# Optimization experiments

Hardware: AMD Instinct MI355X
Metric: run time of the kernel (lower is better)

## Reference

```python
import jax, jax.numpy as jnp
import numpy as np

K = 16          # neighbors per node
EPS = 1e-5      # BatchNorm eps
BN_SCALE = 1.0 / np.sqrt(1.0 + EPS)  # eval BN with running mean=0, var=1


def _knn_idx(x, k):
    # x: [B, N, d] -> idx [B, N, k] of k nearest neighbors (self excluded)
    sq = jnp.sum(x * x, axis=-1)                               # [B, N]
    d2 = sq[:, :, None] + sq[:, None, :] - 2.0 * jnp.einsum('bnd,bmd->bnm', x, x)
    n = x.shape[1]
    d2 = jnp.where(jnp.eye(n, dtype=bool)[None], jnp.inf, d2)  # no self loops
    _, idx = jax.lax.top_k(-d2, k)
    return idx


def _edge_conv(x, idx, W, b, g, be):
    # PyG EdgeConv: max_j MLP([x_i, x_j - x_i]); MLP = Linear+BN(eval)+ReLU
    xj = jax.vmap(lambda xb, ib: xb[ib])(x, idx)               # [B, N, k, d]
    xi = x[:, :, None, :]
    m = jnp.concatenate([jnp.broadcast_to(xi, xj.shape), xj - xi], axis=-1)
    h = m @ W + b                                              # [B, N, k, out]
    h = g * (h * BN_SCALE) + be                                # eval BatchNorm
    h = jax.nn.relu(h)
    return jnp.max(h, axis=2)                                  # scatter-max over k


def setup_inputs() -> dict:
    key = jax.random.key(0)
    ks = jax.random.split(key, 16)
    B, N, D, C = 128, 256, 6, 12

    def w(k_, shape, fan_in):
        return (jax.random.normal(k_, shape, jnp.float32) / np.sqrt(fan_in)).astype(jnp.float32)

    inp = {
        'x':   jax.random.normal(ks[0], (B, N, D), jnp.float32),
        'W1':  w(ks[1], (2 * 6, 64), 12),   'b1': jnp.zeros((64,), jnp.float32),
        'g1':  jnp.ones((64,), jnp.float32), 'be1': jnp.zeros((64,), jnp.float32),
        'W2':  w(ks[2], (2 * 64, 128), 128), 'b2': jnp.zeros((128,), jnp.float32),
        'g2':  jnp.ones((128,), jnp.float32), 'be2': jnp.zeros((128,), jnp.float32),
        'W3':  w(ks[3], (2 * 128, 256), 256), 'b3': jnp.zeros((256,), jnp.float32),
        'g3':  jnp.ones((256,), jnp.float32), 'be3': jnp.zeros((256,), jnp.float32),
        'Wf1': w(ks[4], (256, 128), 256),    'bf1': jnp.zeros((128,), jnp.float32),
        'gf':  jnp.ones((128,), jnp.float32), 'bef': jnp.zeros((128,), jnp.float32),
        'Wf2': w(ks[5], (128, C), 128),      'bf2': jnp.zeros((C,), jnp.float32),
    }
    return inp


def reference(x, W1, b1, g1, be1, W2, b2, g2, be2, W3, b3, g3, be3,
              Wf1, bf1, gf, bef, Wf2, bf2):
    h = _edge_conv(x, _knn_idx(x, K), W1, b1, g1, be1)   # [B, N, 64]
    h = _edge_conv(h, _knn_idx(h, K), W2, b2, g2, be2)   # [B, N, 128]
    h = _edge_conv(h, _knn_idx(h, K), W3, b3, g3, be3)   # [B, N, 256]
    p = jnp.max(h, axis=1)                               # global_max_pool [B, 256]
    f = jax.nn.relu(gf * ((p @ Wf1 + bf1) * BN_SCALE) + bef)
    return f @ Wf2 + bf2                                 # [B, num_classes]
```

## Files before the change

### kernel.cpp

```cpp
#include <hip/hip_runtime.h>
#include <cstdint>
#include <cstddef>

#define KNN 16
#define NPTS 256
#define NBATCH 128

static constexpr float BN_SCALE_F = 0.9999950000374997f;

__device__ inline unsigned int f32_ord(float f) {
    unsigned int u = __float_as_uint(f);
    return (u & 0x80000000u) ? ~u : (u | 0x80000000u);
}

__device__ __forceinline__ int wmap(int n) { return n + 4 * (n >> 4); }

template<int D>
__global__ __launch_bounds__(256) void sq_kernel(const float* __restrict__ x,
                                                 float* __restrict__ sq) {
    const int t = blockIdx.x * 256 + threadIdx.x;
    const float* r = x + (size_t)t * D;
    float s = 0.f;
    #pragma unroll
    for (int d = 0; d < D; ++d) s = fmaf(r[d], r[d], s);
    sq[t] = s;
}

template<int D>
__global__ __launch_bounds__(256) void knn_fused_kernel(
        const float* __restrict__ x, const float* __restrict__ sq,
        int* __restrict__ idx) {
    constexpr int KS = (D >= 16) ? 16 : D;
    constexpr int NSTEP = D / KS;
    constexpr int NLOADG = (128 * KS + 255) / 256;
    const int t  = threadIdx.x;
    const int tx = t & 15, ty = t >> 4;
    const int sr = t >> 1, sc = t & 1;
    const int b  = blockIdx.x >> 1;
    const int i0 = (blockIdx.x & 1) * 128;
    const int base = b * NPTS;

    __shared__ float As[2][KS][132];
    __shared__ float Bs[2][KS][132];
    __shared__ float d2L[128][132];
    __shared__ unsigned char Mi[128][36];

    float4 pa[2], pb[2];
    float  pas[NLOADG], pbs[NLOADG];
    if constexpr (D % 16 == 0) {
        #pragma unroll
        for (int u = 0; u < 2; ++u) {
            const int e = t + u * 256, r = e >> 2, cq = (e & 3) * 4;
            pa[u] = *(const float4*)(x + (size_t)(base + i0 + r) * D + cq);
            pb[u] = *(const float4*)(x + (size_t)(base + r) * D + cq);
        }
    } else {
        #pragma unroll
        for (int u = 0; u < NLOADG; ++u) {
            const int e = t + u * 256;
            if (e < 128 * KS) {
                const int r = e / KS, c = e % KS;
                pas[u] = x[(size_t)(base + i0 + r) * D + c];
                pbs[u] = x[(size_t)(base + r) * D + c];
            }
        }
    }

    float sqi[8];
    #pragma unroll
    for (int m = 0; m < 8; ++m) sqi[m] = sq[base + i0 + ty * 8 + m];

    unsigned int Lv[16], Li[16];
    #pragma unroll
    for (int q = 0; q < 16; ++q) { Lv[q] = 0xFFFFFFFFu; Li[q] = 0u; }

    for (int jt = 0; jt < 2; ++jt) {
        const int j0 = jt * 128;
        float acc[8][8] = {};
        for (int s = 0; s < NSTEP; ++s) {
            const int g   = jt * NSTEP + s;
            const int buf = g & 1;
            if constexpr (D % 16 == 0) {
                #pragma unroll
                for (int u = 0; u < 2; ++u) {
                    const int e = t + u * 256, r = e >> 2, cq = (e & 3) * 4;
                    As[buf][cq + 0][r] = pa[u].x; As[buf][cq + 1][r] = pa[u].y;
                    As[buf][cq + 2][r] = pa[u].z; As[buf][cq + 3][r] = pa[u].w;
                    Bs[buf][cq + 0][r] = pb[u].x; Bs[buf][cq + 1][r] = pb[u].y;
                    Bs[buf][cq + 2][r] = pb[u].z; Bs[buf][cq + 3][r] = pb[u].w;
                }
            } else {
                #pragma unroll
                for (int u = 0; u < NLOADG; ++u) {
                    const int e = t + u * 256;
                    if (e < 128 * KS) {
                        const int r = e / KS, c = e % KS;
                        As[buf][c][r] = pas[u];
                        Bs[buf][c][r] = pbs[u];
                    }
                }
            }

            {
                const int gn2 = g + 1;
                const int njt = gn2 / NSTEP, ns = gn2 % NSTEP;
                if (njt < 2) {
                    if constexpr (D % 16 == 0) {
                        #pragma unroll
                        for (int u = 0; u < 2; ++u) {
                            const int e = t + u * 256, r = e >> 2, cq = (e & 3) * 4;
                            pa[u] = *(const float4*)(x + (size_t)(base + i0 + r) * D
                                                     + ns * KS + cq);
                            pb[u] = *(const float4*)(x + (size_t)(base + njt * 128 + r) * D
                                                     + ns * KS + cq);
                        }
                    } else {
                        #pragma unroll
                        for (int u = 0; u < NLOADG; ++u) {
                            const int e = t + u * 256;
                            if (e < 128 * KS) {
                                const int r = e / KS, c = e % KS;
                                pas[u] = x[(size_t)(base + i0 + r) * D + c];
                                pbs[u] = x[(size_t)(base + njt * 128 + r) * D + c];
                            }
                        }
                    }
                }
            }

            __syncthreads();

            #pragma unroll
            for (int kk = 0; kk < KS; ++kk) {
                float am[8], bm[8];
                *(float4*)&am[0] = *(const float4*)&As[buf][kk][ty * 8];
                *(float4*)&am[4] = *(const float4*)&As[buf][kk][ty * 8 + 4];
                *(float4*)&bm[0] = *(const float4*)&Bs[buf][kk][tx * 4];
                *(float4*)&bm[4] = *(const float4*)&Bs[buf][kk][64 + tx * 4];
                #pragma unroll
                for (int m = 0; m < 8; ++m)
                    #pragma unroll
                    for (int n = 0; n < 8; ++n)
                        acc[m][n] = fmaf(am[m], bm[n], acc[m][n]);
            }
        }

        float sqj[8];
        #pragma unroll
        for (int n = 0; n < 4; ++n) {
            sqj[n]     = sq[base + j0 + tx * 4 + n];
            sqj[n + 4] = sq[base + j0 + 64 + tx * 4 + n];
        }
        #pragma unroll
        for (int m = 0; m < 8; ++m) {
            const int gi = i0 + ty * 8 + m;
            float o0[4], o1[4];
            #pragma unroll
            for (int n = 0; n < 4; ++n) {
                float v0 = (sqi[m] + sqj[n])     - 2.f * acc[m][n];
                float v1 = (sqi[m] + sqj[n + 4]) - 2.f * acc[m][n + 4];
                if (gi == j0 + tx * 4 + n)      v0 = INFINITY;
                if (gi == j0 + 64 + tx * 4 + n) v1 = INFINITY;
                o0[n] = v0; o1[n] = v1;
            }
            *(float4*)&d2L[ty * 8 + m][tx * 4]      = make_float4(o0[0], o0[1], o0[2], o0[3]);
            *(float4*)&d2L[ty * 8 + m][64 + tx * 4] = make_float4(o1[0], o1[1], o1[2], o1[3]);
        }
        __syncthreads();

        #pragma unroll 4
        for (int i = 0; i < 64; ++i) {
            const unsigned int v = f32_ord(d2L[sr][sc * 64 + i]);
            const unsigned int j = (unsigned int)(j0 + sc * 64 + i);
            #pragma unroll
            for (int q = 15; q >= 1; --q) {
                const bool a = v < Lv[q];
                const bool c = v < Lv[q - 1];
                Lv[q] = a ? (c ? Lv[q - 1] : v) : Lv[q];
                Li[q] = a ? (c ? Li[q - 1] : j) : Li[q];
            }
            const bool a0 = v < Lv[0];
            Lv[0] = a0 ? v : Lv[0];
            Li[0] = a0 ? j : Li[0];
        }
    }

    __syncthreads();
    #pragma unroll
    for (int q = 0; q < 16; ++q) {
        d2L[sr][sc * 16 + q] = __uint_as_float(Lv[q]);
        Mi[sr][sc * 16 + q]  = (unsigned char)Li[q];
    }
    __syncthreads();

    if (t < 128) {
        const int row = t;
        int h[2];
        unsigned int cv[2], ci[2];
        #pragma unroll
        for (int c = 0; c < 2; ++c) {
            h[c]  = 0;
            cv[c] = __float_as_uint(d2L[row][c * 16]);
            ci[c] = Mi[row][c * 16];
        }
        int outj[16];
        #pragma unroll
        for (int rd = 0; rd < 16; ++rd) {
            const bool tk = (cv[1] < cv[0]) | ((cv[1] == cv[0]) & (ci[1] < ci[0]));
            const int bc = tk ? 1 : 0;
            outj[rd] = (int)(tk ? ci[1] : ci[0]);
            #pragma unroll
            for (int c = 0; c < 2; ++c) {
                if (c == bc) {
                    const int hn = h[c] + 1;
                    h[c] = hn;
                    if (hn < 16) {
                        cv[c] = __float_as_uint(d2L[row][c * 16 + hn]);
                        ci[c] = Mi[row][c * 16 + hn];
                    } else {
                        cv[c] = 0xFFFFFFFFu;
                    }
                }
            }
        }
        int4* op = (int4*)(idx + (size_t)(base + i0 + row) * KNN);
        op[0] = make_int4(outj[0],  outj[1],  outj[2],  outj[3]);
        op[1] = make_int4(outj[4],  outj[5],  outj[6],  outj[7]);
        op[2] = make_int4(outj[8],  outj[9],  outj[10], outj[11]);
        op[3] = make_int4(outj[12], outj[13], outj[14], outj[15]);
    }
}

template<int D, int C>
__global__ __launch_bounds__(256) void mlp_gemm_kernel(
        const float* __restrict__ x, const float* __restrict__ W,
        const float* __restrict__ bias, const float* __restrict__ g,
        const float* __restrict__ be,
        float* __restrict__ A, float* __restrict__ Bv) {
    constexpr int BM = 128;
    constexpr int KT = (D >= 16) ? 16 : D;
    const int t  = threadIdx.x;
    const int m0 = blockIdx.x * BM;
    const int n0 = blockIdx.y * 128;
    const int tx = t & 15;
    const int ty = t >> 4;

    __shared__ float Xs[KT][BM + 4];
    __shared__ float Ws[KT][160];

    float acc[8][8] = {};

    for (int k0 = 0; k0 < D; k0 += KT) {
        if constexpr (D % 16 == 0) {
            const int r  = t >> 1;
            const int cq = (t & 1) * 8;
            const float* src = x + (size_t)(m0 + r) * D + k0 + cq;
            const float4 v0 = *(const float4*)(src);
            const float4 v1 = *(const float4*)(src + 4);
            Xs[cq + 0][r] = v0.x; Xs[cq + 1][r] = v0.y;
            Xs[cq + 2][r] = v0.z; Xs[cq + 3][r] = v0.w;
            Xs[cq + 4][r] = v1.x; Xs[cq + 5][r] = v1.y;
            Xs[cq + 6][r] = v1.z; Xs[cq + 7][r] = v1.w;
        } else {
            for (int e = t; e < BM * KT; e += 256) {
                const int r = e / KT, c = e % KT;
                Xs[c][r] = x[(size_t)(m0 + r) * D + k0 + c];
            }
        }
        if constexpr (D % 16 == 0) {
            const int wk = t >> 4;
            const int nq = (t & 15) * 8;
            const int mb = wmap(nq);
            const int gn = n0 + nq;
            const int kr = k0 + wk;
            if (gn < C) {
                const float* pt = W + (size_t)kr * C + gn;
                const float* pb = W + (size_t)(D + kr) * C + gn;
                const float4 t0 = *(const float4*)(pt);
                const float4 t1 = *(const float4*)(pt + 4);
                const float4 b0 = *(const float4*)(pb);
                const float4 b1 = *(const float4*)(pb + 4);
                *(float4*)&Ws[wk][mb]     = make_float4(t0.x - b0.x, t0.y - b0.y,
                                                        t0.z - b0.z, t0.w - b0.w);
                *(float4*)&Ws[wk][mb + 4] = make_float4(t1.x - b1.x, t1.y - b1.y,
                                                        t1.z - b1.z, t1.w - b1.w);
            } else {
                const float* pb = W + (size_t)(D + kr) * C + (gn - C);
                *(float4*)&Ws[wk][mb]     = *(const float4*)(pb);
                *(float4*)&Ws[wk][mb + 4] = *(const float4*)(pb + 4);
            }
        } else {
            for (int e = t; e < KT * 128; e += 256) {
                const int k = e >> 7, n = e & 127;
                const int gn = n0 + n, kr = k0 + k;
                Ws[k][wmap(n)] = (gn < C)
                    ? W[(size_t)kr * C + gn] - W[(size_t)(D + kr) * C + gn]
                    : W[(size_t)(D + kr) * C + (gn - C)];
            }
        }
        __syncthreads();

        const int mc = wmap(tx * 8);
        #pragma unroll
        for (int kk = 0; kk < KT; ++kk) {
            float xm[8], wn[8];
            *(float4*)&xm[0] = *(const float4*)&Xs[kk][ty * 8];
            *(float4*)&xm[4] = *(const float4*)&Xs[kk][ty * 8 + 4];
            *(float4*)&wn[0] = *(const float4*)&Ws[kk][mc];
            *(float4*)&wn[4] = *(const float4*)&Ws[kk][mc + 4];
            #pragma unroll
            for (int m = 0; m < 8; ++m)
                #pragma unroll
                for (int n = 0; n < 8; ++n)
                    acc[m][n] = fmaf(xm[m], wn[n], acc[m][n]);
        }
        __syncthreads();
    }

    const int gn = n0 + tx * 8;
    if (gn < C) {
        float fac[8];
        #pragma unroll
        for (int e = 0; e < 8; ++e) fac[e] = g[gn + e] * BN_SCALE_F;
        #pragma unroll
        for (int m = 0; m < 8; ++m) {
            float o[8];
            #pragma unroll
            for (int e = 0; e < 8; ++e) o[e] = fac[e] * acc[m][e];
            float* dst = A + (size_t)(m0 + ty * 8 + m) * C + gn;
            *(float4*)(dst)     = make_float4(o[0], o[1], o[2], o[3]);
            *(float4*)(dst + 4) = make_float4(o[4], o[5], o[6], o[7]);
        }
    } else {
        const int cb = gn - C;
        float fac[8], bb[8], bee[8];
        #pragma unroll
        for (int e = 0; e < 8; ++e) {
            fac[e] = g[cb + e] * BN_SCALE_F;
            bb[e]  = bias[cb + e];
            bee[e] = be[cb + e];
        }
        #pragma unroll
        for (int m = 0; m < 8; ++m) {
            float o[8];
            #pragma unroll
            for (int e = 0; e < 8; ++e)
                o[e] = fmaf(fac[e], acc[m][e] + bb[e], bee[e]);
            float* dst = Bv + (size_t)(m0 + ty * 8 + m) * C + cb;
            *(float4*)(dst)     = make_float4(o[0], o[1], o[2], o[3]);
            *(float4*)(dst + 4) = make_float4(o[4], o[5], o[6], o[7]);
        }
    }
}

template<int C>
__global__ __launch_bounds__(C) void combine_kernel(
        const float* A, const float* __restrict__ Bv,
        const int* __restrict__ idx, float* out) {
    const int bi = blockIdx.x;
    const int c  = threadIdx.x;
    __shared__ int nbr[KNN];
    if (c < KNN) nbr[c] = idx[(size_t)bi * KNN + c];
    __syncthreads();
    const int b0 = bi & ~255;
    float mx = -INFINITY;
    #pragma unroll
    for (int kk = 0; kk < KNN; ++kk)
        mx = fmaxf(mx, Bv[(size_t)(b0 + nbr[kk]) * C + c]);
    float a = A[(size_t)bi * C + c];
    out[(size_t)bi * C + c] = fmaxf(a + mx, 0.f);
}

__global__ __launch_bounds__(256) void head_kernel(
        const float* __restrict__ h3, const float* __restrict__ Wf1,
        const float* __restrict__ bf1, const float* __restrict__ gf,
        const float* __restrict__ bef, const float* __restrict__ Wf2,
        const float* __restrict__ bf2, float* __restrict__ out) {
    const int b   = blockIdx.x;
    const int tid = threadIdx.x;
    __shared__ float p[256];
    __shared__ float f[128];
    const float* hb = h3 + (size_t)b * NPTS * 256;
    float mx = -INFINITY;
    for (int n = 0; n < NPTS; ++n) mx = fmaxf(mx, hb[(size_t)n * 256 + tid]);
    p[tid] = mx;
    __syncthreads();
    if (tid < 128) {
        float acc = bf1[tid];
        for (int d = 0; d < 256; ++d)
            acc = fmaf(p[d], Wf1[(size_t)d * 128 + tid], acc);
        float v = gf[tid] * (acc * BN_SCALE_F) + bef[tid];
        f[tid] = fmaxf(v, 0.f);
    }
    __syncthreads();
    if (tid < 12) {
        float acc = bf2[tid];
        for (int d = 0; d < 128; ++d)
            acc = fmaf(f[d], Wf2[(size_t)d * 12 + tid], acc);
        out[(size_t)b * 12 + tid] = acc;
    }
}

extern "C" void kernel_launch(void* const* d_in, const int* in_sizes, int n_in,
                              void* d_out, int out_size, void* d_ws, size_t ws_size,
                              hipStream_t stream) {
    const float* x   = (const float*)d_in[0];
    const float* W1  = (const float*)d_in[1];
    const float* b1  = (const float*)d_in[2];
    const float* g1  = (const float*)d_in[3];
    const float* be1 = (const float*)d_in[4];
    const float* W2  = (const float*)d_in[5];
    const float* b2  = (const float*)d_in[6];
    const float* g2  = (const float*)d_in[7];
    const float* be2 = (const float*)d_in[8];
    const float* W3  = (const float*)d_in[9];
    const float* b3  = (const float*)d_in[10];
    const float* g3  = (const float*)d_in[11];
    const float* be3 = (const float*)d_in[12];
    const float* Wf1 = (const float*)d_in[13];
    const float* bf1 = (const float*)d_in[14];
    const float* gf  = (const float*)d_in[15];
    const float* bef = (const float*)d_in[16];
    const float* Wf2 = (const float*)d_in[17];
    const float* bf2 = (const float*)d_in[18];
    float* out = (float*)d_out;

    char* ws = (char*)d_ws;
    const size_t idx_bytes = (size_t)NBATCH * NPTS * KNN * sizeof(int);
    const size_t reg_bytes = (size_t)NBATCH * NPTS * 256 * sizeof(float);
    int*   idx = (int*)ws;
    float* R1  = (float*)(ws + idx_bytes);
    float* R2  = (float*)(ws + idx_bytes + reg_bytes);
    float* R3  = (float*)(ws + idx_bytes + 2 * reg_bytes);
    float* sqb = (float*)(ws + idx_bytes + 3 * reg_bytes);

    const int BN = NBATCH * NPTS;
    const int KNN_GRID = NBATCH * 2;
    const int MB = BN / 128;

    sq_kernel<6><<<BN / 256, 256, 0, stream>>>(x, sqb);
    knn_fused_kernel<6><<<KNN_GRID, 256, 0, stream>>>(x, sqb, idx);
    mlp_gemm_kernel<6, 64><<<dim3(MB, 1), 256, 0, stream>>>(
        x, W1, b1, g1, be1, R1, R2);
    combine_kernel<64><<<BN, 64, 0, stream>>>(R1, R2, idx, R1);

    sq_kernel<64><<<BN / 256, 256, 0, stream>>>(R1, sqb);
    knn_fused_kernel<64><<<KNN_GRID, 256, 0, stream>>>(R1, sqb, idx);
    mlp_gemm_kernel<64, 128><<<dim3(MB, 2), 256, 0, stream>>>(
        R1, W2, b2, g2, be2, R2, R3);
    combine_kernel<128><<<BN, 128, 0, stream>>>(R2, R3, idx, R2);

    sq_kernel<128><<<BN / 256, 256, 0, stream>>>(R2, sqb);
    knn_fused_kernel<128><<<KNN_GRID, 256, 0, stream>>>(R2, sqb, idx);
    mlp_gemm_kernel<128, 256><<<dim3(MB, 4), 256, 0, stream>>>(
        R2, W3, b3, g3, be3, R3, R1);
    combine_kernel<256><<<BN, 256, 0, stream>>>(R3, R1, idx, R3);

    head_kernel<<<NBATCH, 256, 0, stream>>>(R3, Wf1, bf1, gf, bef, Wf2, bf2, out);
}
```

Measured before the change: 450.4 us.

## Double-buffer shared tiles with register prefetch in edge-MLP GEMM

The edge-MLP GEMM now keeps two shared-memory buffers for the X and W tiles. It loads the next K-slice from global memory into registers while the current slice is being computed, which overlaps global load latency with FMA work and removes one barrier per K step. It also adds a minimum-occupancy hint of 4 blocks to the launch bounds. The extra prefetch registers and the occupancy hint could raise register pressure or cause spills next to the 64-float accumulator tile. Shared memory use roughly doubles.

```diff
diff --git a/kernel.cpp b/kernel.cpp
--- a/kernel.cpp
+++ b/kernel.cpp
@@ -232,93 +232,157 @@
 }
 
 template<int D, int C>
-__global__ __launch_bounds__(256) void mlp_gemm_kernel(
+__global__ __launch_bounds__(256, 4) void mlp_gemm_kernel(
         const float* __restrict__ x, const float* __restrict__ W,
         const float* __restrict__ bias, const float* __restrict__ g,
         const float* __restrict__ be,
         float* __restrict__ A, float* __restrict__ Bv) {
     constexpr int BM = 128;
     constexpr int KT = (D >= 16) ? 16 : D;
+    constexpr int NSTEP = D / KT;
+    constexpr int NXG = (BM * KT + 255) / 256;
+    constexpr int NWG = (KT * 128 + 255) / 256;
     const int t  = threadIdx.x;
+    const int tx = t & 15;
+    const int ty = t >> 4;
     const int m0 = blockIdx.x * BM;
     const int n0 = blockIdx.y * 128;
-    const int tx = t & 15;
-    const int ty = t >> 4;
-
-    __shared__ float Xs[KT][BM + 4];
-    __shared__ float Ws[KT][160];
+
+    __shared__ float Xs[2][KT][132];
+    __shared__ float Ws[2][KT][164];
 
     float acc[8][8] = {};
 
-    for (int k0 = 0; k0 < D; k0 += KT) {
+    const int xr = t >> 1, xc = (t & 1) * 8;
+    const int wk = t >> 4, nq = (t & 15) * 8;
+    const int gn = n0 + nq;
+    const bool isTop = (gn < C);
+    const int wcol = isTop ? gn : (gn - C);
+    const int mb = wmap(nq);
+
+    float4 px0, px1;
+    float4 wt0, wt1, wb0, wb1;
+    float  pxg[NXG], pwg[NWG];
+
+    if constexpr (D % 16 == 0) {
+        const float* xp = x + (size_t)(m0 + xr) * D + xc;
+        px0 = *(const float4*)(xp);
+        px1 = *(const float4*)(xp + 4);
+        const float* pT = W + (size_t)wk * C + wcol;
+        const float* pB = W + (size_t)(D + wk) * C + wcol;
+        wt0 = *(const float4*)(pT); wt1 = *(const float4*)(pT + 4);
+        wb0 = *(const float4*)(pB); wb1 = *(const float4*)(pB + 4);
+    } else {
+        #pragma unroll
+        for (int u = 0; u < NXG; ++u) {
+            const int e = t + u * 256;
+            if (e < BM * KT) {
+                const int r = e / KT, c = e % KT;
+                pxg[u] = x[(size_t)(m0 + r) * D + c];
+            }
+        }
+        #pragma unroll
+        for (int u = 0; u < NWG; ++u) {
+            const int e = t + u * 256;
+            if (e < KT * 128) {
+                const int k = e >> 7, n = e & 127;
+                const int g2 = n0 + n;
+                pwg[u] = (g2 < C)
+                    ? W[(size_t)k * C + g2] - W[(size_t)(D + k) * C + g2]
+                    : W[(size_t)(D + k) * C + (g2 - C)];
+            }
+        }
+    }
+
+    for (int s = 0; s < NSTEP; ++s) {
+        const int buf = s & 1;
         if constexpr (D % 16 == 0) {
-            const int r  = t >> 1;
-            const int cq = (t & 1) * 8;
-            const float* src = x + (size_t)(m0 + r) * D + k0 + cq;
-            const float4 v0 = *(const float4*)(src);
-            const float4 v1 = *(const float4*)(src + 4);
-            Xs[cq + 0][r] = v0.x; Xs[cq + 1][r] = v0.y;
-            Xs[cq + 2][r] = v0.z; Xs[cq + 3][r] = v0.w;
-            Xs[cq + 4][r] = v1.x; Xs[cq + 5][r] = v1.y;
-            Xs[cq + 6][r] = v1.z; Xs[cq + 7][r] = v1.w;
+            Xs[buf][xc + 0][xr] = px0.x; Xs[buf][xc + 1][xr] = px0.y;
+            Xs[buf][xc + 2][xr] = px0.z; Xs[buf][xc + 3][xr] = px0.w;
+            Xs[buf][xc + 4][xr] = px1.x; Xs[buf][xc + 5][xr] = px1.y;
+            Xs[buf][xc + 6][xr] = px1.z; Xs[buf][xc + 7][xr] = px1.w;
+            float4 v0, v1;
+            if (isTop) {
+                v0 = make_float4(wt0.x - wb0.x, wt0.y - wb0.y,
+                                 wt0.z - wb0.z, wt0.w - wb0.w);
+                v1 = make_float4(wt1.x - wb1.x, wt1.y - wb1.y,
+                                 wt1.z - wb1.z, wt1.w - wb1.w);
+            } else {
+                v0 = wb0; v1 = wb1;
+            }
+            *(float4*)&Ws[buf][wk][mb]     = v0;
+            *(float4*)&Ws[buf][wk][mb + 4] = v1;
         } else {
-            for (int e = t; e < BM * KT; e += 256) {
-                const int r = e / KT, c = e % KT;
-                Xs[c][r] = x[(size_t)(m0 + r) * D + k0 + c];
-            }
-        }
-        if constexpr (D % 16 == 0) {
-            const int wk = t >> 4;
-            const int nq = (t & 15) * 8;
-            const int mb = wmap(nq);
-            const int gn = n0 + nq;
-            const int kr = k0 + wk;
-            if (gn < C) {
-                const float* pt = W + (size_t)kr * C + gn;
-                const float* pb = W + (size_t)(D + kr) * C + gn;
-                const float4 t0 = *(const float4*)(pt);
-                const float4 t1 = *(const float4*)(pt + 4);
-                const float4 b0 = *(const float4*)(pb);
-                const float4 b1 = *(const float4*)(pb + 4);
-                *(float4*)&Ws[wk][mb]     = make_float4(t0.x - b0.x, t0.y - b0.y,
-                                                        t0.z - b0.z, t0.w - b0.w);
-                *(float4*)&Ws[wk][mb + 4] = make_float4(t1.x - b1.x, t1.y - b1.y,
-                                                        t1.z - b1.z, t1.w - b1.w);
+            #pragma unroll
+            for (int u = 0; u < NXG; ++u) {
+                const int e = t + u * 256;
+                if (e < BM * KT) {
+                    const int r = e / KT, c = e % KT;
+                    Xs[buf][c][r] = pxg[u];
+                }
+            }
+            #pragma unroll
+            for (int u = 0; u < NWG; ++u) {
+                const int e = t + u * 256;
+                if (e < KT * 128) {
+                    const int k = e >> 7, n = e & 127;
+                    Ws[buf][k][wmap(n)] = pwg[u];
+                }
+            }
+        }
+
+        if (s + 1 < NSTEP) {
+            const int k0n = (s + 1) * KT;
+            if constexpr (D % 16 == 0) {
+                const float* xp = x + (size_t)(m0 + xr) * D + k0n + xc;
+                px0 = *(const float4*)(xp);
+                px1 = *(const float4*)(xp + 4);
+                const float* pT = W + (size_t)(k0n + wk) * C + wcol;
+                const float* pB = W + (size_t)(D + k0n + wk) * C + wcol;
+                wt0 = *(const float4*)(pT); wt1 = *(const float4*)(pT + 4);
+                wb0 = *(const float4*)(pB); wb1 = *(const float4*)(pB + 4);
             } else {
-                const float* pb = W + (size_t)(D + kr) * C + (gn - C);
-                *(float4*)&Ws[wk][mb]     = *(const float4*)(pb);
-                *(float4*)&Ws[wk][mb + 4] = *(const float4*)(pb + 4);
-            }
-        } else {
-            for (int e = t; e < KT * 128; e += 256) {
-                const int k = e >> 7, n = e & 127;
-                const int gn = n0 + n, kr = k0 + k;
-                Ws[k][wmap(n)] = (gn < C)
-                    ? W[(size_t)kr * C + gn] - W[(size_t)(D + kr) * C + gn]
-                    : W[(size_t)(D + kr) * C + (gn - C)];
-            }
-        }
+                #pragma unroll
+                for (int u = 0; u < NXG; ++u) {
+                    const int e = t + u * 256;
+                    if (e < BM * KT) {
+                        const int r = e / KT, c = e % KT;
+                        pxg[u] = x[(size_t)(m0 + r) * D + k0n + c];
+                    }
+                }
+                #pragma unroll
+                for (int u = 0; u < NWG; ++u) {
+                    const int e = t + u * 256;
+                    if (e < KT * 128) {
+                        const int k = e >> 7, n = e & 127;
+                        const int g2 = n0 + n;
+                        pwg[u] = (g2 < C)
+                            ? W[(size_t)(k0n + k) * C + g2] - W[(size_t)(D + k0n + k) * C + g2]
+                            : W[(size_t)(D + k0n + k) * C + (g2 - C)];
+                    }
+                }
+            }
+        }
+
         __syncthreads();
 
         const int mc = wmap(tx * 8);
         #pragma unroll
         for (int kk = 0; kk < KT; ++kk) {
             float xm[8], wn[8];
-            *(float4*)&xm[0] = *(const float4*)&Xs[kk][ty * 8];
-            *(float4*)&xm[4] = *(const float4*)&Xs[kk][ty * 8 + 4];
-            *(float4*)&wn[0] = *(const float4*)&Ws[kk][mc];
-            *(float4*)&wn[4] = *(const float4*)&Ws[kk][mc + 4];
+            *(float4*)&xm[0] = *(const float4*)&Xs[buf][kk][ty * 8];
+            *(float4*)&xm[4] = *(const float4*)&Xs[buf][kk][ty * 8 + 4];
+            *(float4*)&wn[0] = *(const float4*)&Ws[buf][kk][mc];
+            *(float4*)&wn[4] = *(const float4*)&Ws[buf][kk][mc + 4];
             #pragma unroll
             for (int m = 0; m < 8; ++m)
                 #pragma unroll
                 for (int n = 0; n < 8; ++n)
                     acc[m][n] = fmaf(xm[m], wn[n], acc[m][n]);
         }
-        __syncthreads();
-    }
-
-    const int gn = n0 + tx * 8;
-    if (gn < C) {
+    }
+
+    if (isTop) {
         float fac[8];
         #pragma unroll
         for (int e = 0; e < 8; ++e) fac[e] = g[gn + e] * BN_SCALE_F;
```

Measured after the change: 579.9 us. 28.8% more time.
